# Kernel tuning notes

Measured on AMD Instinct MI355X. Metric: run time of the kernel, lower is better.

## Reference

```python
import jax, jax.numpy as jnp
import numpy as np

B, T, D, H, C = 256, 256, 512, 1024, 128  # batch, steps, input_size, hidden, num_classes


def setup_inputs() -> dict:
    key = jax.random.key(0)
    ks = jax.random.split(key, 8)
    gru_inputs = jax.random.normal(ks[0], (B, T, D), dtype=jnp.float32)
    true_ids = jax.random.randint(ks[1], (B, T), 0, C)
    true_seq = jax.nn.one_hot(true_ids, C, dtype=jnp.float32)
    s = 1.0 / np.sqrt(H).astype(np.float32)
    W_ih = jax.random.uniform(ks[2], (3 * H, D + C), jnp.float32, -s, s)
    b_ih = jax.random.uniform(ks[3], (3 * H,), jnp.float32, -s, s)
    W_hh = jax.random.uniform(ks[4], (3 * H, H), jnp.float32, -s, s)
    b_hh = jax.random.uniform(ks[5], (3 * H,), jnp.float32, -s, s)
    W_out = jax.random.uniform(ks[6], (C, H), jnp.float32, -s, s)
    b_out = jax.random.uniform(ks[7], (C,), jnp.float32, -s, s)
    return {"gru_inputs": gru_inputs, "true_seq": true_seq, "W_ih": W_ih,
            "b_ih": b_ih, "W_hh": W_hh, "b_hh": b_hh, "W_out": W_out, "b_out": b_out}


def reference(gru_inputs, true_seq, W_ih, b_ih, W_hh, b_hh, W_out, b_out):
    # Teacher-forcing (training) branch of TerminalGRU, dropout=0, bos_idx=None.
    Bb, Tt, _ = gru_inputs.shape
    Cc = true_seq.shape[-1]
    Hh = W_hh.shape[1]
    # prev_y[t] = true_seq[t-1], prev_y[0] = zeros (no BOS)
    prev_y = jnp.concatenate(
        [jnp.zeros((Bb, 1, Cc), gru_inputs.dtype), true_seq[:, :-1]], axis=1)
    inp = jnp.concatenate([gru_inputs, prev_y], axis=-1)  # (B,T,D+C)
    # Precompute input-side gate projections as one big GEMM (faithful math).
    gates_x = jnp.einsum('btd,gd->btg', inp, W_ih) + b_ih  # (B,T,3H)
    xr, xz, xn = jnp.split(gates_x, 3, axis=-1)

    def step(h, xs):
        xr_t, xz_t, xn_t = xs  # each (B,H)
        gh = h @ W_hh.T + b_hh  # (B,3H)
        hr, hz, hn = jnp.split(gh, 3, axis=-1)
        r = jax.nn.sigmoid(xr_t + hr)
        z = jax.nn.sigmoid(xz_t + hz)
        n = jnp.tanh(xn_t + r * hn)
        h_new = (1.0 - z) * n + z * h
        return h_new, h_new

    h0 = jnp.zeros((Bb, Hh), gru_inputs.dtype)
    xs = (xr.transpose(1, 0, 2), xz.transpose(1, 0, 2), xn.transpose(1, 0, 2))
    _, hs = jax.lax.scan(step, h0, xs)  # hs: (T,B,H)
    logits = jnp.einsum('tbh,ch->btc', hs, W_out) + b_out  # (B,T,C)
    return logits
```

## Files before the change

kernel.cpp:

```cpp
#include <hip/hip_runtime.h>


#define DEVI __device__ __forceinline__

typedef __bf16 bf16x8 __attribute__((ext_vector_type(8)));
typedef float f32x4 __attribute__((ext_vector_type(4)));
typedef unsigned long long u64;

static constexpr int Bb = 256, Tt = 256, Dd = 512, Hh = 1024, Cc = 128;
static constexpr int G3 = 3072, DC = 640, TC = 32, NC = Tt / TC;
static constexpr int SLOTS = TC + 1;

DEVI unsigned short f2b(float f) {
  union { float f; unsigned u; } v; v.f = f;
  unsigned r = v.u + 0x7FFFu + ((v.u >> 16) & 1u);
  return (unsigned short)(r >> 16);
}
DEVI float b2f(unsigned short h) {
  union { unsigned u; float f; } v; v.u = ((unsigned)h) << 16; return v.f;
}

union HB { unsigned short s[8]; bf16x8 v; };


__global__ __launch_bounds__(256) void k_cvt(const float* __restrict__ x,
                                             unsigned short* __restrict__ o, int n) {
  int i = (blockIdx.x * 256 + threadIdx.x) * 8;
  if (i >= n) return;
  float4 a = *(const float4*)(x + i), b = *(const float4*)(x + i + 4);
  uint4 u;
  u.x = (unsigned)f2b(a.x) | ((unsigned)f2b(a.y) << 16);
  u.y = (unsigned)f2b(a.z) | ((unsigned)f2b(a.w) << 16);
  u.z = (unsigned)f2b(b.x) | ((unsigned)f2b(b.y) << 16);
  u.w = (unsigned)f2b(b.z) | ((unsigned)f2b(b.w) << 16);
  *(uint4*)(o + i) = u;
}

__global__ __launch_bounds__(256) void k_cvt_wa(const float* __restrict__ Wih,
                                                unsigned short* __restrict__ Wa) {
  int u = blockIdx.x * 256 + threadIdx.x;
  int g = u >> 6, d = (u & 63) * 8;
  const float* p = Wih + (size_t)g * DC + d;
  float4 a = *(const float4*)p, b = *(const float4*)(p + 4);
  uint4 o;
  o.x = (unsigned)f2b(a.x) | ((unsigned)f2b(a.y) << 16);
  o.y = (unsigned)f2b(a.z) | ((unsigned)f2b(a.w) << 16);
  o.z = (unsigned)f2b(b.x) | ((unsigned)f2b(b.y) << 16);
  o.w = (unsigned)f2b(b.z) | ((unsigned)f2b(b.w) << 16);
  *(uint4*)(Wa + (size_t)g * Dd + d) = o;
}

__global__ __launch_bounds__(256) void k_cvt_wct(const float* __restrict__ Wih,
                                                 unsigned short* __restrict__ WcT) {
  int g = blockIdx.x * 256 + threadIdx.x;
  int c = blockIdx.y;
  WcT[(size_t)c * G3 + g] = f2b(Wih[(size_t)g * DC + Dd + c]);
}

__global__ __launch_bounds__(256) void k_pid(const float* __restrict__ ts,
                                             int* __restrict__ pid) {
  int bt = blockIdx.x * 256 + threadIdx.x;
  int t = bt & (Tt - 1);
  if (t == 0) { pid[bt] = -1; return; }
  const float* p = ts + (size_t)(bt - 1) * Cc;
  int id = 0;
  for (int c = 0; c < Cc; c += 4) {
    float4 v = *(const float4*)(p + c);
    if (v.x > 0.5f) id = c;
    if (v.y > 0.5f) id = c + 1;
    if (v.z > 0.5f) id = c + 2;
    if (v.w > 0.5f) id = c + 3;
  }
  pid[bt] = id;
}

DEVI bf16x8 ld_a_f32(const float* __restrict__ X, int m, int t0c, int k) {
  int b = m >> 5, tl = m & 31;
  const float* p = X + ((size_t)(b * Tt + t0c + tl)) * Dd + k;
  float4 x = *(const float4*)p, y = *(const float4*)(p + 4);
  HB r;
  r.s[0] = f2b(x.x); r.s[1] = f2b(x.y); r.s[2] = f2b(x.z); r.s[3] = f2b(x.w);
  r.s[4] = f2b(y.x); r.s[5] = f2b(y.y); r.s[6] = f2b(y.z); r.s[7] = f2b(y.w);
  return r.v;
}

DEVI void gates_tile(int mi, int ni, const float* __restrict__ X,
                     const unsigned short* __restrict__ Wa,
                     const unsigned short* __restrict__ WcT,
                     const float* __restrict__ bih,
                     const int* __restrict__ pid,
                     unsigned short* __restrict__ gx, int t0c) {
  int m0 = mi * 128, n0 = ni * 128;
  int l = threadIdx.x & 63, w = threadIdx.x >> 6;
  int wm = w >> 1, wn = w & 1;
  int r0 = m0 + 64 * wm, c0 = n0 + 64 * wn;
  int lr = l & 15, lk = (l >> 4) * 8;
  f32x4 acc[4][4] = {};
  for (int kk = 0; kk < 16; ++kk) {
    int k = kk * 32 + lk;
    bf16x8 a[4], b[4];
#pragma unroll
    for (int mf = 0; mf < 4; ++mf)
      a[mf] = ld_a_f32(X, r0 + 16 * mf + lr, t0c, k);
#pragma unroll
    for (int nf = 0; nf < 4; ++nf)
      b[nf] = *(const bf16x8*)(Wa + (size_t)(c0 + 16 * nf + lr) * Dd + k);
#pragma unroll
    for (int mf = 0; mf < 4; ++mf)
#pragma unroll
      for (int nf = 0; nf < 4; ++nf)
        acc[mf][nf] = __builtin_amdgcn_mfma_f32_16x16x32_bf16(a[mf], b[nf], acc[mf][nf], 0, 0, 0);
  }
  int ri = (l >> 4) * 4;
  for (int mf = 0; mf < 4; ++mf) {
    int rowb = r0 + 16 * mf + ri;
    int pd[4];
#pragma unroll
    for (int i = 0; i < 4; ++i) {
      int rr = rowb + i;
      pd[i] = pid[(size_t)(rr >> 5) * Tt + t0c + (rr & 31)];
    }
    for (int nf = 0; nf < 4; ++nf) {
      int g = c0 + 16 * nf + lr;
      float bi = bih[g];
#pragma unroll
      for (int i = 0; i < 4; ++i) {
        float v = acc[mf][nf][i] + bi;
        if (pd[i] >= 0) v += b2f(WcT[(size_t)pd[i] * G3 + g]);
        gx[(size_t)(rowb + i) * G3 + g] = f2b(v);
      }
    }
  }
}

__global__ __launch_bounds__(256) void k_gatesF(const float* __restrict__ X,
                                                const unsigned short* __restrict__ Wa,
                                                const unsigned short* __restrict__ WcT,
                                                const float* __restrict__ bih,
                                                const int* __restrict__ pid,
                                                unsigned short* __restrict__ gx, int t0c) {
  gates_tile(blockIdx.x, blockIdx.y, X, Wa, WcT, bih, pid, gx, t0c);
}

DEVI void logits_tile(int blk, const unsigned short* __restrict__ hsc,
                      const unsigned short* __restrict__ Wo,
                      const float* __restrict__ bout,
                      float* __restrict__ out, int t0) {
  int l = threadIdx.x & 63, w = threadIdx.x >> 6;
  int lr = l & 15, lk = (l >> 4) * 8;
  int r0 = blk * 64 + 16 * w;
  f32x4 acc[8] = {};
  for (int kk = 0; kk < 32; ++kk) {
    int k = kk * 32 + lk;
    bf16x8 a = *(const bf16x8*)(hsc + (size_t)(r0 + lr) * Hh + k);
#pragma unroll
    for (int nf = 0; nf < 8; ++nf) {
      bf16x8 b = *(const bf16x8*)(Wo + (size_t)(16 * nf + lr) * Hh + k);
      acc[nf] = __builtin_amdgcn_mfma_f32_16x16x32_bf16(a, b, acc[nf], 0, 0, 0);
    }
  }
  int ri = (l >> 4) * 4;
  for (int nf = 0; nf < 8; ++nf) {
    int c = 16 * nf + lr;
    float bo = bout[c];
#pragma unroll
    for (int i = 0; i < 4; ++i) {
      int m = r0 + ri + i;
      int grow = (m >> 5) * Tt + t0 + (m & 31);
      out[(size_t)grow * Cc + c] = acc[nf][i] + bo;
    }
  }
}

__global__ __launch_bounds__(256) void k_combo(
    const float* __restrict__ X, const unsigned short* __restrict__ Wa,
    const unsigned short* __restrict__ WcT, const float* __restrict__ bih,
    const int* __restrict__ pid, unsigned short* __restrict__ gxNext, int doGates,
    const unsigned short* __restrict__ hsc, const unsigned short* __restrict__ Wob,
    const float* __restrict__ bou, float* __restrict__ outp, int t0) {
  int bid = blockIdx.x;
  if (bid < 1536) {
    if (doGates)
      gates_tile(bid & 63, bid >> 6, X, Wa, WcT, bih, pid, gxNext, t0 + TC);
  } else {
    logits_tile(bid - 1536, hsc, Wob, bou, outp, t0);
  }
}

__global__ __launch_bounds__(256, 1) void k_scan(const unsigned short* __restrict__ Whh,
                                                 const float* __restrict__ bhh,
                                                 const unsigned short* __restrict__ gx,
                                                 unsigned short* __restrict__ hring,
                                                 unsigned short* __restrict__ hsc,
                                                 unsigned int* __restrict__ notify,
                                                 int t0) {
  __shared__ float red[4 * 32 * 100];
  const int tid = threadIdx.x;
  const int l = tid & 63, w = tid >> 6;
  const int bid = blockIdx.x;
  const int mg = bid & 7, cb = bid >> 3;
  const int lr = l & 15, lk = (l >> 4) * 8;
  const int hcolBase = 32 * cb;
  const int ri = (l >> 4) * 4;

  bf16x8 Breg[6][8];
#pragma unroll
  for (int nf = 0; nf < 6; ++nf) {
    int wrow = (nf >> 1) * Hh + hcolBase + (nf & 1) * 16 + lr;
#pragma unroll
    for (int kk = 0; kk < 8; ++kk) {
      int k = 256 * w + 32 * kk + lk;
      Breg[nf][kk] = *(const bf16x8*)(Whh + (size_t)wrow * Hh + k);
    }
  }

  const int erow = tid >> 3, ej0 = (tid & 7) * 4;
  const int eb = 32 * mg + erow;
  const int ecol = hcolBase + ej0;
  const float4 bhr4 = *(const float4*)(bhh + ecol);
  const float4 bhz4 = *(const float4*)(bhh + Hh + ecol);
  const float4 bhn4 = *(const float4*)(bhh + 2 * Hh + ecol);

  u64 hsave = 0;

  for (int tl = 0; tl < TC; ++tl) {
    const int t = t0 + tl;
    const unsigned short* hcur = hring + (size_t)(t % SLOTS) * (Bb * Hh);
    u64* hnq = (u64*)hring + (size_t)((t + 1) % SLOTS) * (Bb * Hh / 4);

    const size_t gxo = (size_t)(eb * TC + tl) * G3;
    uint2 gr = *(const uint2*)(gx + gxo + ecol);
    uint2 gz = *(const uint2*)(gx + gxo + Hh + ecol);
    uint2 gn = *(const uint2*)(gx + gxo + 2 * Hh + ecol);

    if (t > 0) {
      const unsigned int* np = notify + (mg << 6) + (l & 31);
      for (;;) {
        unsigned int v = __hip_atomic_load(np, __ATOMIC_RELAXED,
                                           __HIP_MEMORY_SCOPE_AGENT);
        if (__all((int)(v >= (unsigned)t))) break;
      }
    }
    asm volatile("" ::: "memory");

    u64 hprev = (tl == 0) ? *(const u64*)(hcur + (size_t)eb * Hh + ecol) : hsave;

    f32x4 acc[2][6] = {};
#pragma unroll
    for (int kk = 0; kk < 8; ++kk) {
      int k = 256 * w + 32 * kk + lk;
      bf16x8 a[2];
#pragma unroll
      for (int mf = 0; mf < 2; ++mf)
        a[mf] = *(const bf16x8*)(hcur + (size_t)(32 * mg + 16 * mf + lr) * Hh + k);
#pragma unroll
      for (int mf = 0; mf < 2; ++mf)
#pragma unroll
        for (int nf = 0; nf < 6; ++nf)
          acc[mf][nf] = __builtin_amdgcn_mfma_f32_16x16x32_bf16(a[mf], Breg[nf][kk], acc[mf][nf], 0, 0, 0);
    }

#pragma unroll
    for (int mf = 0; mf < 2; ++mf)
#pragma unroll
      for (int nf = 0; nf < 6; ++nf)
#pragma unroll
        for (int i = 0; i < 4; ++i)
          red[(w * 32 + 16 * mf + ri + i) * 100 + (nf >> 1) * 32 + (nf & 1) * 16 + lr] = acc[mf][nf][i];
    __syncthreads();

    f32x4 vr = {}, vz = {}, vn = {};
#pragma unroll
    for (int w2 = 0; w2 < 4; ++w2) {
      const float* rp = &red[(w2 * 32 + erow) * 100];
      vr += *(const f32x4*)(rp + ej0);
      vz += *(const f32x4*)(rp + 32 + ej0);
      vn += *(const f32x4*)(rp + 64 + ej0);
    }
    unsigned short grs[4] = {(unsigned short)gr.x, (unsigned short)(gr.x >> 16),
                             (unsigned short)gr.y, (unsigned short)(gr.y >> 16)};
    unsigned short gzs[4] = {(unsigned short)gz.x, (unsigned short)(gz.x >> 16),
                             (unsigned short)gz.y, (unsigned short)(gz.y >> 16)};
    unsigned short gns[4] = {(unsigned short)gn.x, (unsigned short)(gn.x >> 16),
                             (unsigned short)gn.y, (unsigned short)(gn.y >> 16)};
    u64 ho = 0;
#pragma unroll
    for (int i = 0; i < 4; ++i) {
      float hr = vr[i] + (&bhr4.x)[i];
      float hz = vz[i] + (&bhz4.x)[i];
      float hn = vn[i] + (&bhn4.x)[i];
      float xr = b2f(grs[i]), xz = b2f(gzs[i]), xn = b2f(gns[i]);
      float rg = 1.f / (1.f + __expf(-(xr + hr)));
      float zg = 1.f / (1.f + __expf(-(xz + hz)));
      float pre = xn + rg * hn;
      pre = fminf(fmaxf(pre, -15.f), 15.f);
      float e = __expf(-2.f * pre);
      float ng = (1.f - e) / (1.f + e);
      float hp = b2f((unsigned short)(hprev >> (16 * i)));
      float hv = (1.f - zg) * ng + zg * hp;
      ho |= (u64)f2b(hv) << (16 * i);
    }
    __hip_atomic_store(hnq + ((size_t)eb * Hh + ecol) / 4, ho,
                       __ATOMIC_RELAXED, __HIP_MEMORY_SCOPE_AGENT);
    hsave = ho;

    asm volatile("s_waitcnt vmcnt(0)" ::: "memory");
    __syncthreads();
    if (tid == 0)
      __hip_atomic_store(notify + (mg << 6) + cb, (unsigned)(t + 1),
                         __ATOMIC_RELAXED, __HIP_MEMORY_SCOPE_AGENT);
    *(u64*)(hsc + (size_t)(eb * TC + tl) * Hh + ecol) = ho;
  }
}

extern "C" void kernel_launch(void* const* d_in, const int* in_sizes, int n_in,
                              void* d_out, int out_size, void* d_ws, size_t ws_size,
                              hipStream_t stream) {
  const float* gru = (const float*)d_in[0];
  const float* ts  = (const float*)d_in[1];
  const float* Wih = (const float*)d_in[2];
  const float* bih = (const float*)d_in[3];
  const float* Whh = (const float*)d_in[4];
  const float* bhh = (const float*)d_in[5];
  const float* Wou = (const float*)d_in[6];
  const float* bou = (const float*)d_in[7];
  float* out = (float*)d_out;

  char* ws = (char*)d_ws;
  size_t off = 0;
  auto alloc = [&](size_t bytes) -> void* {
    void* p = ws + off;
    off += (bytes + 255) & ~(size_t)255;
    return p;
  };
  unsigned short* Wa    = (unsigned short*)alloc((size_t)G3 * Dd * 2);
  unsigned short* WcT   = (unsigned short*)alloc((size_t)Cc * G3 * 2);
  unsigned short* Whb   = (unsigned short*)alloc((size_t)G3 * Hh * 2);
  unsigned short* Wob   = (unsigned short*)alloc((size_t)Cc * Hh * 2);
  int*            pid   = (int*)alloc((size_t)Bb * Tt * 4);
  unsigned short* hring = (unsigned short*)alloc((size_t)SLOTS * Bb * Hh * 2);
  unsigned int*   nfy   = (unsigned int*)alloc((size_t)8 * 64 * 4);
  unsigned short* gxb0  = (unsigned short*)alloc((size_t)Bb * TC * G3 * 2);
  unsigned short* gxb1  = (unsigned short*)alloc((size_t)Bb * TC * G3 * 2);
  unsigned short* hsc   = (unsigned short*)alloc((size_t)Bb * TC * Hh * 2);
  if (ws_size < off) return;
  unsigned short* gxb[2] = { gxb0, gxb1 };

  k_cvt<<<(G3 * Hh) / 2048, 256, 0, stream>>>(Whh, Whb, G3 * Hh);
  k_cvt<<<(Cc * Hh) / 2048, 256, 0, stream>>>(Wou, Wob, Cc * Hh);
  k_cvt_wa<<<(G3 * 64) / 256, 256, 0, stream>>>(Wih, Wa);
  k_cvt_wct<<<dim3(G3 / 256, Cc), 256, 0, stream>>>(Wih, WcT);
  k_pid<<<(Bb * Tt) / 256, 256, 0, stream>>>(ts, pid);
  hipMemsetAsync(hring, 0, (size_t)Bb * Hh * 2, stream);
  hipMemsetAsync(nfy, 0, (size_t)8 * 64 * 4, stream);

  k_gatesF<<<dim3(64, 24), 256, 0, stream>>>(gru, Wa, WcT, bih, pid, gxb[0], 0);

  for (int c = 0; c < NC; ++c) {
    int t0 = c * TC;
    k_scan<<<dim3(256), dim3(256), 0, stream>>>(Whb, bhh, gxb[c & 1], hring, hsc, nfy, t0);
    k_combo<<<dim3(1664), dim3(256), 0, stream>>>(
        gru, Wa, WcT, bih, pid, gxb[(c + 1) & 1], (c + 1 < NC) ? 1 : 0,
        hsc, Wob, bou, out, t0);
  }
}
```

Baseline: 2.810 ms.

## Fold next-chunk input-gate GEMM into recurrent scan kernel time steps

The input-gate projection for the next time chunk moves out of the separate combo kernel and into the persistent scan kernel. Each block computes three k-slices of a gates tile after every recurrent step, so the MFMA work fills idle time spent waiting on the cross-block notify barrier. The logits GEMM becomes its own small kernel. The cost is extra register pressure in the scan kernel, which already holds the W_hh fragments, and extra work on the serial critical path of each step.

```diff
diff --git a/kernel.cpp b/kernel.cpp
--- a/kernel.cpp
+++ b/kernel.cpp
@@ -84,12 +84,12 @@
   return r.v;
 }
 
-DEVI void gates_tile(int mi, int ni, const float* __restrict__ X,
-                     const unsigned short* __restrict__ Wa,
-                     const unsigned short* __restrict__ WcT,
-                     const float* __restrict__ bih,
-                     const int* __restrict__ pid,
-                     unsigned short* __restrict__ gx, int t0c) {
+DEVI void gates_tile_f32(int mi, int ni, const float* __restrict__ X,
+                         const unsigned short* __restrict__ Wa,
+                         const unsigned short* __restrict__ WcT,
+                         const float* __restrict__ bih,
+                         const int* __restrict__ pid,
+                         unsigned short* __restrict__ gx, int t0c) {
   int m0 = mi * 128, n0 = ni * 128;
   int l = threadIdx.x & 63, w = threadIdx.x >> 6;
   int wm = w >> 1, wn = w & 1;
@@ -139,13 +139,14 @@
                                                 const float* __restrict__ bih,
                                                 const int* __restrict__ pid,
                                                 unsigned short* __restrict__ gx, int t0c) {
-  gates_tile(blockIdx.x, blockIdx.y, X, Wa, WcT, bih, pid, gx, t0c);
-}
-
-DEVI void logits_tile(int blk, const unsigned short* __restrict__ hsc,
-                      const unsigned short* __restrict__ Wo,
-                      const float* __restrict__ bout,
-                      float* __restrict__ out, int t0) {
+  gates_tile_f32(blockIdx.x, blockIdx.y, X, Wa, WcT, bih, pid, gx, t0c);
+}
+
+__global__ __launch_bounds__(256) void k_logits(const unsigned short* __restrict__ hsc,
+                                                const unsigned short* __restrict__ Wo,
+                                                const float* __restrict__ bout,
+                                                float* __restrict__ out, int t0) {
+  int blk = blockIdx.x;
   int l = threadIdx.x & 63, w = threadIdx.x >> 6;
   int lr = l & 15, lk = (l >> 4) * 8;
   int r0 = blk * 64 + 16 * w;
@@ -172,28 +173,13 @@
   }
 }
 
-__global__ __launch_bounds__(256) void k_combo(
-    const float* __restrict__ X, const unsigned short* __restrict__ Wa,
+__global__ __launch_bounds__(256, 1) void k_scan(
+    const unsigned short* __restrict__ Whh, const float* __restrict__ bhh,
+    const unsigned short* __restrict__ gx, unsigned short* __restrict__ hring,
+    unsigned short* __restrict__ hsc, unsigned int* __restrict__ notify, int t0,
+    const float* __restrict__ gruX, const unsigned short* __restrict__ Wa,
     const unsigned short* __restrict__ WcT, const float* __restrict__ bih,
-    const int* __restrict__ pid, unsigned short* __restrict__ gxNext, int doGates,
-    const unsigned short* __restrict__ hsc, const unsigned short* __restrict__ Wob,
-    const float* __restrict__ bou, float* __restrict__ outp, int t0) {
-  int bid = blockIdx.x;
-  if (bid < 1536) {
-    if (doGates)
-      gates_tile(bid & 63, bid >> 6, X, Wa, WcT, bih, pid, gxNext, t0 + TC);
-  } else {
-    logits_tile(bid - 1536, hsc, Wob, bou, outp, t0);
-  }
-}
-
-__global__ __launch_bounds__(256, 1) void k_scan(const unsigned short* __restrict__ Whh,
-                                                 const float* __restrict__ bhh,
-                                                 const unsigned short* __restrict__ gx,
-                                                 unsigned short* __restrict__ hring,
-                                                 unsigned short* __restrict__ hsc,
-                                                 unsigned int* __restrict__ notify,
-                                                 int t0) {
+    const int* __restrict__ pid, unsigned short* __restrict__ gxN, int doGates) {
   __shared__ float red[4 * 32 * 100];
   const int tid = threadIdx.x;
   const int l = tid & 63, w = tid >> 6;
@@ -202,6 +188,8 @@
   const int lr = l & 15, lk = (l >> 4) * 8;
   const int hcolBase = 32 * cb;
   const int ri = (l >> 4) * 4;
+  const int wm = w >> 1, wn = w & 1;
+  const int t0n = t0 + TC;
 
   bf16x8 Breg[6][8];
 #pragma unroll
@@ -222,6 +210,7 @@
   const float4 bhn4 = *(const float4*)(bhh + 2 * Hh + ecol);
 
   u64 hsave = 0;
+  f32x4 gacc[4][4] = {};
 
   for (int tl = 0; tl < TC; ++tl) {
     const int t = t0 + tl;
@@ -310,6 +299,55 @@
       __hip_atomic_store(notify + (mg << 6) + cb, (unsigned)(t + 1),
                          __ATOMIC_RELAXED, __HIP_MEMORY_SCOPE_AGENT);
     *(u64*)(hsc + (size_t)(eb * TC + tl) * Hh + ecol) = ho;
+
+    if (doGates) {
+      for (int j = 0; j < 3; ++j) {
+        int u = tl * 3 + j;
+        int tau = bid * 6 + (u >> 4);
+        int kk = u & 15;
+        int mi = tau & 63, ni = tau >> 6;
+        int r0g = mi * 128 + 64 * wm, c0g = ni * 128 + 64 * wn;
+        int kg = kk * 32 + lk;
+        bf16x8 a[4], b[4];
+#pragma unroll
+        for (int mf = 0; mf < 4; ++mf)
+          a[mf] = ld_a_f32(gruX, r0g + 16 * mf + lr, t0n, kg);
+#pragma unroll
+        for (int nf = 0; nf < 4; ++nf)
+          b[nf] = *(const bf16x8*)(Wa + (size_t)(c0g + 16 * nf + lr) * Dd + kg);
+#pragma unroll
+        for (int mf = 0; mf < 4; ++mf)
+#pragma unroll
+          for (int nf = 0; nf < 4; ++nf)
+            gacc[mf][nf] = __builtin_amdgcn_mfma_f32_16x16x32_bf16(a[mf], b[nf], gacc[mf][nf], 0, 0, 0);
+        if (kk == 15) {
+          for (int mf = 0; mf < 4; ++mf) {
+            int rowb = r0g + 16 * mf + ri;
+            int pd[4];
+#pragma unroll
+            for (int i = 0; i < 4; ++i) {
+              int rr = rowb + i;
+              pd[i] = pid[(size_t)(rr >> 5) * Tt + t0n + (rr & 31)];
+            }
+            for (int nf = 0; nf < 4; ++nf) {
+              int g = c0g + 16 * nf + lr;
+              float bi = bih[g];
+#pragma unroll
+              for (int i = 0; i < 4; ++i) {
+                float v = gacc[mf][nf][i] + bi;
+                if (pd[i] >= 0) v += b2f(WcT[(size_t)pd[i] * G3 + g]);
+                gxN[(size_t)(rowb + i) * G3 + g] = f2b(v);
+              }
+            }
+          }
+#pragma unroll
+          for (int mf = 0; mf < 4; ++mf)
+#pragma unroll
+            for (int nf = 0; nf < 4; ++nf)
+              gacc[mf][nf] = f32x4{};
+        }
+      }
+    }
   }
 }
 
@@ -358,9 +396,9 @@
 
   for (int c = 0; c < NC; ++c) {
     int t0 = c * TC;
-    k_scan<<<dim3(256), dim3(256), 0, stream>>>(Whb, bhh, gxb[c & 1], hring, hsc, nfy, t0);
-    k_combo<<<dim3(1664), dim3(256), 0, stream>>>(
-        gru, Wa, WcT, bih, pid, gxb[(c + 1) & 1], (c + 1 < NC) ? 1 : 0,
-        hsc, Wob, bou, out, t0);
-  }
-}
+    k_scan<<<dim3(256), dim3(256), 0, stream>>>(
+        Whb, bhh, gxb[c & 1], hring, hsc, nfy, t0,
+        gru, Wa, WcT, bih, pid, gxb[(c + 1) & 1], (c + 1 < NC) ? 1 : 0);
+    k_logits<<<(Bb * TC) / 64, 256, 0, stream>>>(hsc, Wob, bou, out, t0);
+  }
+}
```

Measured after the change: 3.448 ms. +22.7%, slower.
